# Kernel optimization log

Hardware: AMD Instinct MI355X
Metric: run time of the kernel (lower is better)

The kernel has to match this reference:

```python
import jax, jax.numpy as jnp
import numpy as np

# dims
H = 2048      # hidden_size
NH = 16       # num q heads
NKV = 8       # num kv heads
D = 128       # head_dim
E = 16        # routed experts
K = 4         # top_k
I = 1024      # moe_intermediate_size (per routed expert)
SI = 1024     # shared expert intermediate (moe_intermediate * num_shared)
T = 2048      # tokens
EPS = 1e-5
THETA = 10000.0
RSF = 1.0     # router_scaling_factor


def setup_inputs() -> dict:
    key = jax.random.key(0)
    ks = jax.random.split(key, 10)
    s = 0.02
    return {
        "positions": jnp.arange(T, dtype=jnp.int32),
        "hidden_states": jax.random.normal(ks[0], (T, H), jnp.float32),
        "qkv_w": jax.random.normal(ks[1], (H, (NH + 2 * NKV) * D), jnp.float32) * s,
        "o_w": jax.random.normal(ks[2], (NH * D, H), jnp.float32) * s,
        "q_norm_w": jnp.ones((D,), jnp.float32),
        "k_norm_w": jnp.ones((D,), jnp.float32),
        "ln1_w": jnp.ones((H,), jnp.float32),
        "ln2_w": jnp.ones((H,), jnp.float32),
        "gate_w": jax.random.normal(ks[3], (H, E), jnp.float32) * s,
        "expert_bias": jax.random.normal(ks[4], (E,), jnp.float32) * 0.1,
        "shared_gu_w": jax.random.normal(ks[5], (H, 2 * SI), jnp.float32) * s,
        "shared_down_w": jax.random.normal(ks[6], (SI, H), jnp.float32) * s,
        "exp_gu_w": jax.random.normal(ks[7], (E, H, 2 * I), jnp.float32) * s,
        "exp_down_w": jax.random.normal(ks[8], (E, I, H), jnp.float32) * s,
    }


def _rmsnorm(x, w):
    v = jnp.mean(x * x, axis=-1, keepdims=True)
    return x * jax.lax.rsqrt(v + EPS) * w


def _rope(x, cos, sin):
    # neox style: rotate halves. x: [T, heads, D]; cos/sin: [T, 1, D//2]
    x1, x2 = x[..., : D // 2], x[..., D // 2 :]
    return jnp.concatenate([x1 * cos - x2 * sin, x2 * cos + x1 * sin], axis=-1)


def reference(positions, hidden_states, qkv_w, o_w, q_norm_w, k_norm_w,
              ln1_w, ln2_w, gate_w, expert_bias, shared_gu_w, shared_down_w,
              exp_gu_w, exp_down_w):
    hs = hidden_states
    # --- attention block ---
    x = _rmsnorm(hs, ln1_w)
    qkv = x @ qkv_w
    q = qkv[:, : NH * D].reshape(T, NH, D)
    k = qkv[:, NH * D : NH * D + NKV * D].reshape(T, NKV, D)
    v = qkv[:, NH * D + NKV * D :].reshape(T, NKV, D)
    # per-head qk RMSNorm
    q = _rmsnorm(q, q_norm_w)
    k = _rmsnorm(k, k_norm_w)
    # rotary embedding
    inv_freq = 1.0 / (THETA ** (jnp.arange(0, D, 2, dtype=jnp.float32) / D))
    ang = positions.astype(jnp.float32)[:, None] * inv_freq  # [T, D/2]
    cos = jnp.cos(ang)[:, None, :]
    sin = jnp.sin(ang)[:, None, :]
    q = _rope(q, cos, sin)
    k = _rope(k, cos, sin)
    # GQA: repeat kv heads
    rep = NH // NKV
    k = jnp.repeat(k, rep, axis=1)  # [T, NH, D]
    v = jnp.repeat(v, rep, axis=1)
    scores = jnp.einsum('qhd,khd->hqk', q, k) * (D ** -0.5)
    causal = jnp.tril(jnp.ones((T, T), dtype=bool))
    scores = jnp.where(causal[None], scores, -1e30)
    attn = jax.nn.softmax(scores, axis=-1)
    ao = jnp.einsum('hqk,khd->qhd', attn, v).reshape(T, NH * D)
    h = hs + ao @ o_w
    # --- MoE block ---
    x2 = _rmsnorm(h, ln2_w)
    router_logits = x2 @ gate_w  # fp32 gate
    sig = jax.nn.sigmoid(router_logits)
    biased = sig + expert_bias  # correction bias only used for selection
    _, top_idx = jax.lax.top_k(biased, K)  # [T, K]
    w = jnp.take_along_axis(sig, top_idx, axis=-1)
    w = w / jnp.sum(w, axis=-1, keepdims=True) * RSF  # renormalize + routed scaling
    combine = jnp.sum(jax.nn.one_hot(top_idx, E, dtype=x2.dtype) * w[..., None], axis=1)  # [T, E]
    # routed experts (dense-masked reference for the grouped GEMM)
    gu = jnp.einsum('th,ehi->eti', x2, exp_gu_w)  # [E, T, 2I]
    act = jax.nn.silu(gu[..., :I]) * gu[..., I:]
    routed = jnp.einsum('eti,eih->eth', act, exp_down_w)
    routed = jnp.einsum('eth,te->th', routed, combine)
    # shared expert
    sgu = x2 @ shared_gu_w
    shared = (jax.nn.silu(sgu[:, :SI]) * sgu[:, SI:]) @ shared_down_w
    return h + routed + shared
```

## Files before the change

kernel.cpp:

```cpp
#include <hip/hip_runtime.h>
#include <math.h>

#define T_ 2048
#define H_ 2048
#define NH_ 16
#define NKV_ 8
#define D_ 128
#define E_ 16
#define I_ 1024
#define SI_ 1024

typedef _Float16 half8 __attribute__((ext_vector_type(8)));
typedef _Float16 half4_t __attribute__((ext_vector_type(4)));
typedef float f32x4 __attribute__((ext_vector_type(4)));

#define MFMA32(a,b,c) __builtin_amdgcn_mfma_f32_16x16x32_f16((a),(b),(c),0,0,0)

__device__ __constant__ float LO_S = 2048.0f;
__device__ __constant__ float LO_I = 1.0f/2048.0f;
#define EPS_ 1e-5f

#define GL16(gp, lp) __builtin_amdgcn_global_load_lds( \
    (const __attribute__((address_space(1))) unsigned int*)(const void*)(gp), \
    (__attribute__((address_space(3))) unsigned int*)(void*)(lp), 16, 0, 0)

__global__ void tables_k(const int* __restrict__ pos, float* __restrict__ cosT, float* __restrict__ sinT) {
  int t = blockIdx.x;
  int j = threadIdx.x;
  float pf = (float)pow(10000.0, (double)j / 64.0);
  float invf = 1.0f / pf;
  float ang = (float)pos[t] * invf;
  cosT[t*64 + j] = (float)cos((double)ang);
  sinT[t*64 + j] = (float)sin((double)ang);
}

__global__ __launch_bounds__(256) void rmsnorm_k(const float* __restrict__ x, const float* __restrict__ w,
                                                 _Float16* __restrict__ oh, _Float16* __restrict__ ol) {
  int row = blockIdx.x;
  const float* xr = x + (size_t)row * H_;
  int tid = threadIdx.x;
  float4 a = *(const float4*)(xr + tid*8);
  float4 b = *(const float4*)(xr + tid*8 + 4);
  float ss = a.x*a.x + a.y*a.y + a.z*a.z + a.w*a.w + b.x*b.x + b.y*b.y + b.z*b.z + b.w*b.w;
  #pragma unroll
  for (int m = 1; m < 64; m <<= 1) ss += __shfl_xor(ss, m);
  __shared__ float wsum[4];
  int wid = tid >> 6, lane = tid & 63;
  if (lane == 0) wsum[wid] = ss;
  __syncthreads();
  float tot = wsum[0] + wsum[1] + wsum[2] + wsum[3];
  float rinv = 1.0f / sqrtf(tot / (float)H_ + EPS_);
  const float* av = (const float*)&a;
  const float* bv = (const float*)&b;
  #pragma unroll
  for (int j = 0; j < 8; ++j) {
    float xv = (j < 4) ? av[j] : bv[j-4];
    float val = xv * rinv * w[tid*8 + j];
    _Float16 h = (_Float16)val;
    size_t o = (size_t)row*H_ + tid*8 + j;
    oh[o] = h;
    ol[o] = (_Float16)((val - (float)h) * LO_S);
  }
}

__global__ __launch_bounds__(128) void qkvpost_k(
    const float* __restrict__ qkv, const float* __restrict__ qnw, const float* __restrict__ knw,
    const float* __restrict__ cosT, const float* __restrict__ sinT,
    _Float16* __restrict__ qh, _Float16* __restrict__ ql,
    _Float16* __restrict__ kh, _Float16* __restrict__ kl,
    _Float16* __restrict__ vth, _Float16* __restrict__ vtl) {
  int t = blockIdx.x, u = blockIdx.y, d = threadIdx.x;
  float val = qkv[(size_t)t*4096 + u*128 + d];
  __shared__ float sv[128];
  __shared__ float ssum[2];
  if (u < 24) {
    float ss = val * val;
    #pragma unroll
    for (int m = 1; m < 64; m <<= 1) ss += __shfl_xor(ss, m);
    if ((d & 63) == 0) ssum[d >> 6] = ss;
    __syncthreads();
    float rinv = 1.0f / sqrtf((ssum[0] + ssum[1]) / 128.0f + EPS_);
    const float* nw = (u < 16) ? qnw : knw;
    float nv = val * rinv * nw[d];
    sv[d] = nv;
    __syncthreads();
    int j = d & 63;
    float c = cosT[t*64 + j], s = sinT[t*64 + j];
    float x1 = sv[j], x2 = sv[j + 64];
    float o = (d < 64) ? (x1*c - x2*s) : (x2*c + x1*s);
    _Float16 hv = (_Float16)o;
    _Float16 lv = (_Float16)((o - (float)hv) * LO_S);
    if (u < 16) { size_t off = ((size_t)u*T_ + t)*D_ + d; qh[off] = hv; ql[off] = lv; }
    else { size_t off = ((size_t)(u-16)*T_ + t)*D_ + d; kh[off] = hv; kl[off] = lv; }
  } else {
    int kv = u - 24;
    _Float16 hv = (_Float16)val;
    _Float16 lv = (_Float16)((val - (float)hv) * LO_S);
    size_t off = ((size_t)kv*D_ + d)*T_ + t;
    vth[off] = hv; vtl[off] = lv;
  }
}

template<bool SPL>
__global__ __launch_bounds__(256) void transpose_k(const float* __restrict__ in, _Float16* __restrict__ oh,
                                                   _Float16* __restrict__ ol, int R, int C) {
  size_t zo = (size_t)blockIdx.z * R * C;
  in += zo; oh += zo; if (SPL) ol += zo;
  __shared__ float tile[32][33];
  int c0 = blockIdx.x*32, r0 = blockIdx.y*32;
  int tid = threadIdx.x;
  int lr = tid >> 3;
  int lc = (tid & 7) * 4;
  float4 v = *(const float4*)(in + (size_t)(r0+lr)*C + c0 + lc);
  tile[lr][lc+0]=v.x; tile[lr][lc+1]=v.y; tile[lr][lc+2]=v.z; tile[lr][lc+3]=v.w;
  __syncthreads();
  half4_t hv, lv;
  #pragma unroll
  for (int j = 0; j < 4; ++j) {
    float f = tile[lc+j][lr];
    _Float16 h = (_Float16)f;
    hv[j] = h;
    if (SPL) lv[j] = (_Float16)((f - (float)h) * LO_S);
  }
  size_t ob = (size_t)(c0+lr)*R + r0 + lc;
  *(half4_t*)(oh + ob) = hv;
  if (SPL) *(half4_t*)(ol + ob) = lv;
}

__global__ __launch_bounds__(256) void transpose_gu_k(const float* __restrict__ in, _Float16* __restrict__ out,
                                                      int R, int Ih) {
  size_t zi = (size_t)blockIdx.z * R * 2 * Ih;
  in += zi; out += zi;
  __shared__ float tg[32][17], tu[32][17];
  int j0 = blockIdx.x*16, h0 = blockIdx.y*32;
  int tid = threadIdx.x;
  int lh = tid >> 3;
  int lj = (tid & 7) * 2;
  int C = 2*Ih;
  float2 g = *(const float2*)(in + (size_t)(h0+lh)*C + j0 + lj);
  float2 u = *(const float2*)(in + (size_t)(h0+lh)*C + Ih + j0 + lj);
  tg[lh][lj]=g.x; tg[lh][lj+1]=g.y; tu[lh][lj]=u.x; tu[lh][lj+1]=u.y;
  __syncthreads();
  int orow = tid >> 3;
  int oj = orow >> 1, op = orow & 1;
  int oc = (tid & 7) * 4;
  float (*sel)[17] = op ? tu : tg;
  half4_t pack;
  #pragma unroll
  for (int q = 0; q < 4; ++q) pack[q] = (_Float16)sel[oc+q][oj];
  *(half4_t*)(out + (size_t)(2*(j0+oj)+op)*R + h0 + oc) = pack;
}

__global__ __launch_bounds__(256) void attn_k(
    const _Float16* __restrict__ qh_, const _Float16* __restrict__ ql_,
    const _Float16* __restrict__ kh_, const _Float16* __restrict__ kl_,
    const _Float16* __restrict__ vh_, const _Float16* __restrict__ vl_,
    _Float16* __restrict__ aoh, _Float16* __restrict__ aol) {
  __shared__ _Float16 sK [2][4096];
  __shared__ _Float16 sKl[2][4096];
  __shared__ _Float16 sV [2][4096];
  __shared__ _Float16 sVl[2][4096];
  const int head = blockIdx.x;
  const int pair = blockIdx.y;
  const int kvh = head >> 1;
  const int wid = threadIdx.x >> 6, lane = threadIdx.x & 63;
  const int fr = lane & 15, fs = lane >> 4;
  const float scale = 0.08838834764831845f;

  const char* kbC  = (const char*)(kh_ + (size_t)kvh*T_*D_);
  const char* kbCl = (const char*)(kl_ + (size_t)kvh*T_*D_);
  const char* vbC  = (const char*)(vh_ + (size_t)kvh*D_*T_);
  const char* vbCl = (const char*)(vl_ + (size_t)kvh*D_*T_);

  auto stage = [&](int buf, int kvt) {
    #pragma unroll
    for (int i = 0; i < 2; ++i) {
      const int off  = wid*2048 + i*1024;
      const int loff = off + lane*16;
      const int r  = loff >> 8;
      const int u  = (loff >> 4) & 15;
      const int us = u ^ (r & 7);
      const size_t gb = ((size_t)(kvt + r) << 8) + ((size_t)us << 4);
      GL16(kbC  + gb, (char*)&sK [buf][0] + off);
      GL16(kbCl + gb, (char*)&sKl[buf][0] + off);
      const int d   = loff >> 6;
      const int uv  = (loff >> 4) & 3;
      const int uvs = uv ^ (d & 3);
      const size_t gvb = (size_t)d*(T_*2) + (size_t)kvt*2 + ((size_t)uvs << 4);
      GL16(vbC  + gvb, (char*)&sV [buf][0] + off);
      GL16(vbCl + gvb, (char*)&sVl[buf][0] + off);
    }
  };

  #pragma unroll 1
  for (int halfT = 0; halfT < 2; ++halfT) {
    const int tile = halfT == 0 ? (31 - pair) : pair;
    const int q0 = tile*64 + wid*16;
    const int qrow = q0 + fr;
    const _Float16* qb_  = qh_ + ((size_t)head*T_ + qrow)*D_;
    const _Float16* qlb_ = ql_ + ((size_t)head*T_ + qrow)*D_;
    half8 qf[4], qfl[4];
    #pragma unroll
    for (int s = 0; s < 4; ++s) {
      qf[s]  = *(const half8*)(qb_  + s*32 + fs*8);
      qfl[s] = *(const half8*)(qlb_ + s*32 + fs*8);
    }
    float m = -1e30f, lsum = 0.f;
    f32x4 oacc[8] = {};
    f32x4 oacc2[8] = {};
    const int nc = 2*tile + 2;

    stage(0, 0);
    #pragma unroll 1
    for (int c = 0; c < nc; ++c) {
      const int kvt = c*32;
      const int buf = c & 1;
      __syncthreads();
      if (c + 1 < nc) stage(buf ^ 1, kvt + 32);

      f32x4 sa = {0,0,0,0}, sa2 = {0,0,0,0}, sb = {0,0,0,0}, sb2 = {0,0,0,0};
      __builtin_amdgcn_s_setprio(1);
      #pragma unroll
      for (int s = 0; s < 4; ++s) {
        const int rA = fr, rB = fr + 16;
        const int eA = (((4*s + fs) ^ (rA & 7)) << 3);
        const int eB = (((4*s + fs) ^ (rB & 7)) << 3);
        half8 kfA  = *(const half8*)&sK [buf][rA*128 + eA];
        half8 kflA = *(const half8*)&sKl[buf][rA*128 + eA];
        half8 kfB  = *(const half8*)&sK [buf][rB*128 + eB];
        half8 kflB = *(const half8*)&sKl[buf][rB*128 + eB];
        sa  = MFMA32(kfA, qf[s], sa);
        sa2 = MFMA32(kfA, qfl[s], sa2);
        sa2 = MFMA32(kflA, qf[s], sa2);
        sb  = MFMA32(kfB, qf[s], sb);
        sb2 = MFMA32(kfB, qfl[s], sb2);
        sb2 = MFMA32(kflB, qf[s], sb2);
      }
      __builtin_amdgcn_s_setprio(0);

      float sv[8];
      #pragma unroll
      for (int r = 0; r < 4; ++r) {
        float xA = (sa[r] + sa2[r]*LO_I) * scale;
        sv[r] = (kvt + fs*4 + r > qrow) ? -INFINITY : xA;
        float xB = (sb[r] + sb2[r]*LO_I) * scale;
        sv[4+r] = (kvt + 16 + fs*4 + r > qrow) ? -INFINITY : xB;
      }
      float tm = -INFINITY;
      #pragma unroll
      for (int j = 0; j < 8; ++j) tm = fmaxf(tm, sv[j]);
      tm = fmaxf(tm, __shfl_xor(tm, 16));
      tm = fmaxf(tm, __shfl_xor(tm, 32));
      float mnew = fmaxf(m, tm);
      float p[8]; float ps = 0.f;
      #pragma unroll
      for (int j = 0; j < 8; ++j) { p[j] = __expf(sv[j] - mnew); ps += p[j]; }
      ps += __shfl_xor(ps, 16);
      ps += __shfl_xor(ps, 32);
      if (mnew > m) {
        float f = __expf(m - mnew);
        lsum *= f;
        #pragma unroll
        for (int db = 0; db < 8; ++db) { oacc[db] *= f; oacc2[db] *= f; }
        m = mnew;
      }
      lsum += ps;
      half8 ph, pl;
      #pragma unroll
      for (int j = 0; j < 8; ++j) {
        _Float16 hp = (_Float16)p[j];
        ph[j] = hp;
        pl[j] = (_Float16)((p[j] - (float)hp) * LO_S);
      }

      __builtin_amdgcn_s_setprio(1);
      #pragma unroll
      for (int db = 0; db < 8; ++db) {
        const int d0 = db*16 + fr;
        const int base = d0*32;
        const int e1 = ((((fs>>1)    ) ^ (d0 & 3)) << 3) + (fs & 1)*4;
        const int e2 = (((2 + (fs>>1)) ^ (d0 & 3)) << 3) + (fs & 1)*4;
        half4_t v0  = *(const half4_t*)&sV [buf][base + e1];
        half4_t v1  = *(const half4_t*)&sV [buf][base + e2];
        half4_t v0l = *(const half4_t*)&sVl[buf][base + e1];
        half4_t v1l = *(const half4_t*)&sVl[buf][base + e2];
        half8 vf, vfl;
        #pragma unroll
        for (int j = 0; j < 4; ++j) { vf[j] = v0[j]; vf[4+j] = v1[j]; vfl[j] = v0l[j]; vfl[4+j] = v1l[j]; }
        oacc[db]  = MFMA32(vf, ph, oacc[db]);
        oacc2[db] = MFMA32(vf, pl, oacc2[db]);
        oacc2[db] = MFMA32(vfl, ph, oacc2[db]);
      }
      __builtin_amdgcn_s_setprio(0);
    }
    __syncthreads();

    float inv = 1.0f / lsum;
    #pragma unroll
    for (int db = 0; db < 8; ++db) {
      #pragma unroll
      for (int r = 0; r < 4; ++r) {
        float val = (oacc[db][r] + oacc2[db][r]*LO_I) * inv;
        int dd = db*16 + fs*4 + r;
        size_t off = (size_t)qrow*(NH_*D_) + head*D_ + dd;
        _Float16 hv = (_Float16)val;
        aoh[off] = hv;
        aol[off] = (_Float16)((val - (float)hv) * LO_S);
      }
    }
  }
}

__global__ __launch_bounds__(256) void router_k(const _Float16* __restrict__ x2h, const _Float16* __restrict__ x2l,
    const float* __restrict__ gw, const float* __restrict__ eb,
    int* __restrict__ cnt, int* __restrict__ list, float* __restrict__ wl) {
  int t = blockIdx.x*4 + (threadIdx.x >> 6);
  int lane = threadIdx.x & 63;
  const _Float16* xh = x2h + (size_t)t*H_;
  const _Float16* xl = x2l + (size_t)t*H_;
  f32x4 a0 = {0,0,0,0}, a1 = {0,0,0,0}, a2 = {0,0,0,0}, a3 = {0,0,0,0};
  for (int h = lane; h < H_; h += 64) {
    float xv = (float)xh[h] + (float)xl[h] * LO_I;
    const float* g = gw + (size_t)h*16;
    a0 += xv * (*(const f32x4*)(g));
    a1 += xv * (*(const f32x4*)(g+4));
    a2 += xv * (*(const f32x4*)(g+8));
    a3 += xv * (*(const f32x4*)(g+12));
  }
  float acc[16];
  #pragma unroll
  for (int j = 0; j < 4; ++j) { acc[j]=a0[j]; acc[4+j]=a1[j]; acc[8+j]=a2[j]; acc[12+j]=a3[j]; }
  #pragma unroll
  for (int mm = 1; mm < 64; mm <<= 1) {
    #pragma unroll
    for (int e2 = 0; e2 < 16; ++e2) acc[e2] += __shfl_xor(acc[e2], mm);
  }
  if (lane == 0) {
    float sig[16], biased[16];
    #pragma unroll
    for (int e2 = 0; e2 < 16; ++e2) {
      float s = 1.0f / (1.0f + expf(-acc[e2]));
      sig[e2] = s; biased[e2] = s + eb[e2];
    }
    int sel[4]; float wv[4]; float wsum = 0.f;
    unsigned used = 0;
    for (int j = 0; j < 4; ++j) {
      int bi = -1; float bv = -1e30f;
      for (int e2 = 0; e2 < 16; ++e2)
        if (!((used >> e2) & 1) && biased[e2] > bv) { bv = biased[e2]; bi = e2; }
      used |= 1u << bi;
      sel[j] = bi; wv[j] = sig[bi]; wsum += sig[bi];
    }
    for (int j = 0; j < 4; ++j) {
      int e2 = sel[j];
      int pos = atomicAdd(&cnt[e2], 1);
      list[e2*T_ + pos] = t;
      wl[e2*T_ + pos] = wv[j] / wsum;
    }
  }
}

__global__ void scan_k(const int* __restrict__ cnt, int* __restrict__ base) {
  if (threadIdx.x == 0 && blockIdx.x == 0) {
    int s = 0;
    for (int e2 = 0; e2 < 16; ++e2) { base[e2] = s; s += cnt[e2]; }
  }
}

struct GArgs {
  const _Float16* Ah; const _Float16* Al;
  const _Float16* Bh; const _Float16* Bl;
  int M, N, K;
  const int* rowlist; const float* wlist; const int* cnt; const int* base;
  float* C; const float* res; _Float16* act; float* outAt; int ldc;
};

template<int MODE, bool SPLIT>
__global__ __launch_bounds__(256) void gemm_k(GArgs p) {
  const int e = blockIdx.z;
  const int M = p.cnt ? p.cnt[e] : p.M;
  const int m0 = blockIdx.y * 128;
  if (m0 >= M) return;
  const int n0 = blockIdx.x * 128;
  const int tid = threadIdx.x;
  const int wid = tid >> 6, lane = tid & 63;

  __shared__ _Float16 sA[2][4096];
  __shared__ _Float16 sB[2][4096];
  __shared__ _Float16 sAl[SPLIT ? 2 : 1][SPLIT ? 4096 : 8];
  __shared__ _Float16 sBl[SPLIT ? 2 : 1][SPLIT ? 4096 : 8];

  const char* aPtr[2]; const char* alPtr[2];
  const char* bPtr[2]; const char* blPtr[2];
  int ldsOff[2];
  #pragma unroll
  for (int i = 0; i < 2; ++i) {
    const int u = (i*4 + wid)*64 + lane;
    const int row = u >> 2;
    const int slot = ((u & 3) ^ (row & 3)) * 16;
    ldsOff[i] = (i*4 + wid) * 1024;
    size_t aIdx;
    if constexpr (MODE == 2) {
      if (p.rowlist) {
        int tok = p.rowlist[(size_t)e * T_ + m0 + row];
        tok = tok < 0 ? 0 : (tok > T_ - 1 ? T_ - 1 : tok);
        aIdx = (size_t)tok;
      } else aIdx = (size_t)(m0 + row);
    } else if constexpr (MODE == 3) {
      aIdx = (size_t)p.base[e] + m0 + row;
    } else {
      aIdx = (size_t)(m0 + row);
    }
    aPtr[i] = (const char*)(p.Ah + aIdx * (size_t)p.K) + slot;
    if constexpr (SPLIT) alPtr[i] = (const char*)(p.Al + aIdx * (size_t)p.K) + slot;
    const size_t bIdx = (size_t)e * p.N + n0 + row;
    bPtr[i] = (const char*)(p.Bh + bIdx * (size_t)p.K) + slot;
    if constexpr (SPLIT) blPtr[i] = (const char*)(p.Bl + bIdx * (size_t)p.K) + slot;
  }

  auto stage = [&](int buf, int kb) {
    #pragma unroll
    for (int i = 0; i < 2; ++i) {
      GL16(aPtr[i] + kb, (char*)&sA[buf][0] + ldsOff[i]);
      GL16(bPtr[i] + kb, (char*)&sB[buf][0] + ldsOff[i]);
      if constexpr (SPLIT) {
        GL16(alPtr[i] + kb, (char*)&sAl[buf][0] + ldsOff[i]);
        GL16(blPtr[i] + kb, (char*)&sBl[buf][0] + ldsOff[i]);
      }
    }
  };

  const int wr = (wid >> 1) * 64, wc = (wid & 1) * 64;
  const int fr = lane & 15, fs = lane >> 4;

  f32x4 acc[4][4] = {};
  f32x4 acc2[4][4] = {};

  stage(0, 0);
  __syncthreads();
  int cur = 0;
  for (int k0 = 0; k0 < p.K; k0 += 32) {
    if (k0 + 32 < p.K) stage(cur ^ 1, (k0 + 32) * 2);
    half8 ah[4], bh[4], al[4], bl[4];
    #pragma unroll
    for (int i = 0; i < 4; ++i) {
      const int pa = (fs ^ ((wr + i*16 + fr) & 3)) * 8;
      const int pb = (fs ^ ((wc + i*16 + fr) & 3)) * 8;
      ah[i] = *(const half8*)&sA[cur][(wr + i*16 + fr)*32 + pa];
      bh[i] = *(const half8*)&sB[cur][(wc + i*16 + fr)*32 + pb];
      if constexpr (SPLIT) {
        al[i] = *(const half8*)&sAl[cur][(wr + i*16 + fr)*32 + pa];
        bl[i] = *(const half8*)&sBl[cur][(wc + i*16 + fr)*32 + pb];
      }
    }
    __builtin_amdgcn_s_setprio(1);
    #pragma unroll
    for (int mi = 0; mi < 4; ++mi) {
      #pragma unroll
      for (int ni = 0; ni < 4; ++ni) {
        acc[mi][ni] = MFMA32(ah[mi], bh[ni], acc[mi][ni]);
        if constexpr (SPLIT) {
          acc2[mi][ni] = MFMA32(ah[mi], bl[ni], acc2[mi][ni]);
          acc2[mi][ni] = MFMA32(al[mi], bh[ni], acc2[mi][ni]);
        }
      }
    }
    __builtin_amdgcn_s_setprio(0);
    __syncthreads();
    cur ^= 1;
  }

  const int actld = p.N >> 1;
  #pragma unroll
  for (int mi = 0; mi < 4; ++mi) {
    #pragma unroll
    for (int ni = 0; ni < 4; ++ni) {
      f32x4 v4 = acc[mi][ni];
      if constexpr (SPLIT) v4 = v4 + acc2[mi][ni] * LO_I;
      const int colb = n0 + wc + ni*16 + fr;
      #pragma unroll
      for (int r = 0; r < 4; ++r) {
        const int row = m0 + wr + mi*16 + fs*4 + r;
        float val = v4[r];
        if constexpr (MODE == 0) {
          if (row < M) p.C[(size_t)row * p.ldc + colb] = val;
        } else if constexpr (MODE == 1) {
          if (row < M) p.C[(size_t)row * p.ldc + colb] = p.res[(size_t)row * p.ldc + colb] + val;
        } else if constexpr (MODE == 2) {
          float other = __shfl_xor(val, 1);
          float g = (fr & 1) ? other : val;
          float u = (fr & 1) ? val : other;
          float a = g / (1.0f + expf(-g)) * u;
          if (!(fr & 1) && row < M) {
            size_t ar = (size_t)(p.base ? p.base[e] : 0) + row;
            p.act[ar * (size_t)actld + (colb >> 1)] = (_Float16)a;
          }
        } else {
          if (row < M) {
            int tok = p.rowlist[(size_t)e * T_ + row];
            float w = p.wlist[(size_t)e * T_ + row];
            atomicAdd(&p.outAt[(size_t)tok * p.ldc + colb], val * w);
          }
        }
      }
    }
  }
}

extern "C" void kernel_launch(void* const* d_in, const int* in_sizes, int n_in,
                              void* d_out, int out_size, void* d_ws, size_t ws_size,
                              hipStream_t stream) {
  (void)in_sizes; (void)n_in; (void)out_size; (void)ws_size;
  const int*   positions = (const int*)  d_in[0];
  const float* hidden    = (const float*)d_in[1];
  const float* qkv_w     = (const float*)d_in[2];
  const float* o_w       = (const float*)d_in[3];
  const float* q_norm_w  = (const float*)d_in[4];
  const float* k_norm_w  = (const float*)d_in[5];
  const float* ln1_w     = (const float*)d_in[6];
  const float* ln2_w     = (const float*)d_in[7];
  const float* gate_w    = (const float*)d_in[8];
  const float* ebias     = (const float*)d_in[9];
  const float* sgu_w     = (const float*)d_in[10];
  const float* sdown_w   = (const float*)d_in[11];
  const float* egu_w     = (const float*)d_in[12];
  const float* edown_w   = (const float*)d_in[13];
  float* out = (float*)d_out;

  char* wsp = (char*)d_ws;
  size_t off = 0;
  auto alloc = [&](size_t bytes) -> void* {
    void* p = wsp + off;
    off = (off + bytes + 255) & ~(size_t)255;
    return p;
  };
  float*    cosT   = (float*)   alloc((size_t)T_*64*4);
  float*    sinT   = (float*)   alloc((size_t)T_*64*4);
  _Float16* x_h    = (_Float16*)alloc((size_t)T_*H_*2);
  _Float16* x_l    = (_Float16*)alloc((size_t)T_*H_*2);
  float*    qkvb   = (float*)   alloc((size_t)T_*4096*4);
  _Float16* q_h    = (_Float16*)alloc((size_t)NH_*T_*D_*2);
  _Float16* q_l    = (_Float16*)alloc((size_t)NH_*T_*D_*2);
  _Float16* k_h    = (_Float16*)alloc((size_t)NKV_*T_*D_*2);
  _Float16* k_l    = (_Float16*)alloc((size_t)NKV_*T_*D_*2);
  _Float16* vt_h   = (_Float16*)alloc((size_t)NKV_*T_*D_*2);
  _Float16* vt_l   = (_Float16*)alloc((size_t)NKV_*T_*D_*2);
  _Float16* ao_h   = (_Float16*)alloc((size_t)T_*NH_*D_*2);
  _Float16* ao_l   = (_Float16*)alloc((size_t)T_*NH_*D_*2);
  float*    hbuf   = (float*)   alloc((size_t)T_*H_*4);
  _Float16* x2_h   = (_Float16*)alloc((size_t)T_*H_*2);
  _Float16* x2_l   = (_Float16*)alloc((size_t)T_*H_*2);
  _Float16* qkvwT_h= (_Float16*)alloc((size_t)4096*H_*2);
  _Float16* qkvwT_l= (_Float16*)alloc((size_t)4096*H_*2);
  _Float16* owT_h  = (_Float16*)alloc((size_t)H_*H_*2);
  _Float16* owT_l  = (_Float16*)alloc((size_t)H_*H_*2);
  _Float16* sguT   = (_Float16*)alloc((size_t)2*SI_*H_*2);
  _Float16* sdownT = (_Float16*)alloc((size_t)H_*SI_*2);
  _Float16* eguT   = (_Float16*)alloc((size_t)E_*2*I_*H_*2);
  _Float16* edownT = (_Float16*)alloc((size_t)E_*H_*I_*2);
  _Float16* act_s  = (_Float16*)alloc((size_t)T_*SI_*2);
  _Float16* act_e  = (_Float16*)alloc((size_t)(T_*4 + 128)*I_*2);
  int*   cnt   = (int*)  alloc(E_*4);
  int*   ebase = (int*)  alloc(E_*4);
  int*   list  = (int*)  alloc((size_t)E_*T_*4);
  float* wlst  = (float*)alloc((size_t)E_*T_*4);

  hipMemsetAsync(cnt, 0, E_*4, stream);
  tables_k<<<T_, 64, 0, stream>>>(positions, cosT, sinT);

  transpose_k<true ><<<dim3(4096/32, H_/32, 1), 256, 0, stream>>>(qkv_w, qkvwT_h, qkvwT_l, H_, 4096);
  transpose_k<true ><<<dim3(H_/32,  H_/32, 1), 256, 0, stream>>>(o_w, owT_h, owT_l, H_, H_);
  transpose_gu_k    <<<dim3(SI_/16, H_/32, 1), 256, 0, stream>>>(sgu_w, sguT, H_, SI_);
  transpose_k<false><<<dim3(H_/32, SI_/32, 1), 256, 0, stream>>>(sdown_w, sdownT, nullptr, SI_, H_);
  transpose_gu_k    <<<dim3(I_/16,  H_/32, E_), 256, 0, stream>>>(egu_w, eguT, H_, I_);
  transpose_k<false><<<dim3(H_/32,  I_/32, E_), 256, 0, stream>>>(edown_w, edownT, nullptr, I_, H_);

  rmsnorm_k<<<T_, 256, 0, stream>>>(hidden, ln1_w, x_h, x_l);

  { GArgs g{}; g.Ah=x_h; g.Al=x_l; g.Bh=qkvwT_h; g.Bl=qkvwT_l; g.M=T_; g.N=4096; g.K=H_;
    g.C=qkvb; g.ldc=4096;
    gemm_k<0,true><<<dim3(4096/128, T_/128, 1), 256, 0, stream>>>(g); }

  qkvpost_k<<<dim3(T_, 32, 1), 128, 0, stream>>>(qkvb, q_norm_w, k_norm_w, cosT, sinT,
                                                 q_h, q_l, k_h, k_l, vt_h, vt_l);

  attn_k<<<dim3(NH_, 16), 256, 0, stream>>>(q_h, q_l, k_h, k_l, vt_h, vt_l, ao_h, ao_l);

  { GArgs g{}; g.Ah=ao_h; g.Al=ao_l; g.Bh=owT_h; g.Bl=owT_l; g.M=T_; g.N=H_; g.K=H_;
    g.C=hbuf; g.res=hidden; g.ldc=H_;
    gemm_k<1,true><<<dim3(H_/128, T_/128, 1), 256, 0, stream>>>(g); }

  rmsnorm_k<<<T_, 256, 0, stream>>>(hbuf, ln2_w, x2_h, x2_l);

  router_k<<<T_/4, 256, 0, stream>>>(x2_h, x2_l, gate_w, ebias, cnt, list, wlst);
  scan_k<<<1, 64, 0, stream>>>(cnt, ebase);

  { GArgs g{}; g.Ah=x2_h; g.Bh=sguT; g.M=T_; g.N=2*SI_; g.K=H_; g.act=act_s;
    gemm_k<2,false><<<dim3(2*SI_/128, T_/128, 1), 256, 0, stream>>>(g); }

  { GArgs g{}; g.Ah=act_s; g.Bh=sdownT; g.M=T_; g.N=H_; g.K=SI_;
    g.C=out; g.res=hbuf; g.ldc=H_;
    gemm_k<1,false><<<dim3(H_/128, T_/128, 1), 256, 0, stream>>>(g); }

  { GArgs g{}; g.Ah=x2_h; g.Bh=eguT; g.M=T_; g.N=2*I_; g.K=H_;
    g.rowlist=list; g.cnt=cnt; g.base=ebase; g.act=act_e;
    gemm_k<2,false><<<dim3(2*I_/128, T_/128, E_), 256, 0, stream>>>(g); }

  { GArgs g{}; g.Ah=act_e; g.Bh=edownT; g.M=T_; g.N=H_; g.K=I_;
    g.rowlist=list; g.wlist=wlst; g.cnt=cnt; g.base=ebase;
    g.outAt=out; g.ldc=H_;
    gemm_k<3,false><<<dim3(H_/128, T_/128, E_), 256, 0, stream>>>(g); }
}
```

Baseline: 1.202 ms.

## Add 256x256 tile GEMM for routed experts and tighten pipeline waits

Adds a new 512-thread GEMM kernel with 256x256 output tiles, used for the two routed-expert grouped GEMMs, so each loaded operand is reused across more MFMA work. The existing 128-tile GEMM swaps its plain __syncthreads for explicit vmcnt waits and s_barrier wrapped in sched_barriers, letting the prefetch of the next K-slice stay in flight while the current one is computed. The expert activation buffer padding grows to cover the larger tile overrun. Larger tiles waste more work on partially filled expert tiles and raise register pressure, and the hand-tuned wait counts must match the number of issued loads exactly.

```diff
diff --git a/kernel.cpp b/kernel.cpp
--- a/kernel.cpp
+++ b/kernel.cpp
@@ -437,10 +437,19 @@
   f32x4 acc2[4][4] = {};
 
   stage(0, 0);
-  __syncthreads();
   int cur = 0;
   for (int k0 = 0; k0 < p.K; k0 += 32) {
-    if (k0 + 32 < p.K) stage(cur ^ 1, (k0 + 32) * 2);
+    if (k0 + 32 < p.K) {
+      stage(cur ^ 1, (k0 + 32) * 2);
+      __builtin_amdgcn_sched_barrier(0);
+      asm volatile("s_waitcnt vmcnt(%0)" :: "i"(SPLIT ? 8 : 4) : "memory");
+    } else {
+      __builtin_amdgcn_sched_barrier(0);
+      asm volatile("s_waitcnt vmcnt(0)" ::: "memory");
+    }
+    __builtin_amdgcn_s_barrier();
+    __builtin_amdgcn_sched_barrier(0);
+
     half8 ah[4], bh[4], al[4], bl[4];
     #pragma unroll
     for (int i = 0; i < 4; ++i) {
@@ -466,7 +475,9 @@
       }
     }
     __builtin_amdgcn_s_setprio(0);
-    __syncthreads();
+    __builtin_amdgcn_sched_barrier(0);
+    __builtin_amdgcn_s_barrier();
+    __builtin_amdgcn_sched_barrier(0);
     cur ^= 1;
   }
 
@@ -481,6 +492,137 @@
       #pragma unroll
       for (int r = 0; r < 4; ++r) {
         const int row = m0 + wr + mi*16 + fs*4 + r;
+        float val = v4[r];
+        if constexpr (MODE == 0) {
+          if (row < M) p.C[(size_t)row * p.ldc + colb] = val;
+        } else if constexpr (MODE == 1) {
+          if (row < M) p.C[(size_t)row * p.ldc + colb] = p.res[(size_t)row * p.ldc + colb] + val;
+        } else if constexpr (MODE == 2) {
+          float other = __shfl_xor(val, 1);
+          float g = (fr & 1) ? other : val;
+          float u = (fr & 1) ? val : other;
+          float a = g / (1.0f + expf(-g)) * u;
+          if (!(fr & 1) && row < M) {
+            size_t ar = (size_t)(p.base ? p.base[e] : 0) + row;
+            p.act[ar * (size_t)actld + (colb >> 1)] = (_Float16)a;
+          }
+        } else {
+          if (row < M) {
+            int tok = p.rowlist[(size_t)e * T_ + row];
+            float w = p.wlist[(size_t)e * T_ + row];
+            atomicAdd(&p.outAt[(size_t)tok * p.ldc + colb], val * w);
+          }
+        }
+      }
+    }
+  }
+}
+
+template<int MODE>
+__global__ __launch_bounds__(512) void gemm256_k(GArgs p) {
+  const int e = blockIdx.z;
+  const int M = p.cnt ? p.cnt[e] : p.M;
+  const int m0 = blockIdx.y * 256;
+  if (m0 >= M) return;
+  const int n0 = blockIdx.x * 256;
+  const int tid = threadIdx.x;
+  const int wid = tid >> 6, lane = tid & 63;
+
+  __shared__ _Float16 sA[2][8192];
+  __shared__ _Float16 sB[2][8192];
+
+  const char* aP[2]; const char* bP[2];
+  int ldsO[2];
+  #pragma unroll
+  for (int i = 0; i < 2; ++i) {
+    const int U = i*512 + tid;
+    const int row = U >> 2;
+    const int lu = (U & 3) ^ (row & 3);
+    ldsO[i] = i*8192 + wid*1024;
+    size_t aIdx;
+    if constexpr (MODE == 2) {
+      int tok = p.rowlist[(size_t)e*T_ + m0 + row];
+      tok = tok < 0 ? 0 : (tok > T_-1 ? T_-1 : tok);
+      aIdx = (size_t)tok;
+    } else if constexpr (MODE == 3) {
+      aIdx = (size_t)p.base[e] + m0 + row;
+    } else {
+      aIdx = (size_t)(m0 + row);
+    }
+    aP[i] = (const char*)(p.Ah + aIdx*(size_t)p.K) + lu*16;
+    const size_t bIdx = (size_t)e*p.N + n0 + row;
+    bP[i] = (const char*)(p.Bh + bIdx*(size_t)p.K) + lu*16;
+  }
+
+  auto stage = [&](int buf, int kb) {
+    #pragma unroll
+    for (int i = 0; i < 2; ++i) {
+      GL16(aP[i] + kb, (char*)&sA[buf][0] + ldsO[i]);
+      GL16(bP[i] + kb, (char*)&sB[buf][0] + ldsO[i]);
+    }
+  };
+
+  const int rowb = (wid >> 2) * 128, colb0 = (wid & 3) * 64;
+  const int fr = lane & 15, fs = lane >> 4;
+  int aOff[8], bOff[4];
+  #pragma unroll
+  for (int mi = 0; mi < 8; ++mi) {
+    const int row = rowb + mi*16 + fr;
+    aOff[mi] = row*32 + ((fs ^ (row & 3)) * 8);
+  }
+  #pragma unroll
+  for (int ni = 0; ni < 4; ++ni) {
+    const int row = colb0 + ni*16 + fr;
+    bOff[ni] = row*32 + ((fs ^ (row & 3)) * 8);
+  }
+
+  f32x4 acc[8][4] = {};
+
+  stage(0, 0);
+  int cur = 0;
+  const int nt = p.K >> 5;
+  for (int t = 0; t < nt; ++t) {
+    if (t + 1 < nt) {
+      stage(cur ^ 1, (t + 1) * 64);
+      __builtin_amdgcn_sched_barrier(0);
+      asm volatile("s_waitcnt vmcnt(4)" ::: "memory");
+    } else {
+      __builtin_amdgcn_sched_barrier(0);
+      asm volatile("s_waitcnt vmcnt(0)" ::: "memory");
+    }
+    __builtin_amdgcn_s_barrier();
+    __builtin_amdgcn_sched_barrier(0);
+
+    half8 af[8], bf[4];
+    #pragma unroll
+    for (int ni = 0; ni < 4; ++ni) bf[ni] = *(const half8*)&sB[cur][bOff[ni]];
+    #pragma unroll
+    for (int mi = 0; mi < 8; ++mi) af[mi] = *(const half8*)&sA[cur][aOff[mi]];
+    __builtin_amdgcn_s_setprio(1);
+    #pragma unroll
+    for (int mi = 0; mi < 8; ++mi) {
+      #pragma unroll
+      for (int ni = 0; ni < 4; ++ni) {
+        acc[mi][ni] = MFMA32(af[mi], bf[ni], acc[mi][ni]);
+      }
+    }
+    __builtin_amdgcn_s_setprio(0);
+    __builtin_amdgcn_sched_barrier(0);
+    __builtin_amdgcn_s_barrier();
+    __builtin_amdgcn_sched_barrier(0);
+    cur ^= 1;
+  }
+
+  const int actld = p.N >> 1;
+  #pragma unroll
+  for (int mi = 0; mi < 8; ++mi) {
+    #pragma unroll
+    for (int ni = 0; ni < 4; ++ni) {
+      f32x4 v4 = acc[mi][ni];
+      const int colb = n0 + colb0 + ni*16 + fr;
+      #pragma unroll
+      for (int r = 0; r < 4; ++r) {
+        const int row = m0 + rowb + mi*16 + fs*4 + r;
         float val = v4[r];
         if constexpr (MODE == 0) {
           if (row < M) p.C[(size_t)row * p.ldc + colb] = val;
@@ -559,7 +701,7 @@
   _Float16* eguT   = (_Float16*)alloc((size_t)E_*2*I_*H_*2);
   _Float16* edownT = (_Float16*)alloc((size_t)E_*H_*I_*2);
   _Float16* act_s  = (_Float16*)alloc((size_t)T_*SI_*2);
-  _Float16* act_e  = (_Float16*)alloc((size_t)(T_*4 + 128)*I_*2);
+  _Float16* act_e  = (_Float16*)alloc((size_t)(T_*4 + 512)*I_*2);
   int*   cnt   = (int*)  alloc(E_*4);
   int*   ebase = (int*)  alloc(E_*4);
   int*   list  = (int*)  alloc((size_t)E_*T_*4);
@@ -604,10 +746,10 @@
 
   { GArgs g{}; g.Ah=x2_h; g.Bh=eguT; g.M=T_; g.N=2*I_; g.K=H_;
     g.rowlist=list; g.cnt=cnt; g.base=ebase; g.act=act_e;
-    gemm_k<2,false><<<dim3(2*I_/128, T_/128, E_), 256, 0, stream>>>(g); }
+    gemm256_k<2><<<dim3(2*I_/256, T_/256, E_), 512, 0, stream>>>(g); }
 
   { GArgs g{}; g.Ah=act_e; g.Bh=edownT; g.M=T_; g.N=H_; g.K=I_;
     g.rowlist=list; g.wlist=wlst; g.cnt=cnt; g.base=ebase;
     g.outAt=out; g.ldc=H_;
-    gemm_k<3,false><<<dim3(H_/128, T_/128, E_), 256, 0, stream>>>(g); }
-}
+    gemm256_k<3><<<dim3(H_/256, T_/256, E_), 512, 0, stream>>>(g); }
+}
```

Measured after the change: 1.554 ms. 1.29x slower.
